# Kernel optimization log

Hardware: AMD Instinct MI355X
Metric: run time of the kernel (lower is better)

## Reference

```python
import jax, jax.numpy as jnp
import numpy as np

NEG_SLOPE = 0.2  # PyG GATConv default leaky_relu slope


def gat_conv(x, ei, W, a_src, a_dst, b, heads, ch):
    """One PyG-style GATConv (eval mode, add_self_loops already applied to ei)."""
    N = x.shape[0]
    h = (x @ W).reshape(N, heads, ch)                      # [N,H,C]
    src, dst = ei[0], ei[1]
    al_s = jnp.sum(h * a_src, axis=-1)                     # [N,H]
    al_d = jnp.sum(h * a_dst, axis=-1)                     # [N,H]
    e = jax.nn.leaky_relu(al_s[src] + al_d[dst], NEG_SLOPE)  # [E,H]
    m = jax.ops.segment_max(e, dst, num_segments=N)        # stable softmax over in-edges
    ex = jnp.exp(e - m[dst])
    den = jax.ops.segment_sum(ex, dst, num_segments=N)
    alpha = ex / den[dst]                                  # [E,H]
    msg = alpha[:, :, None] * h[src]                       # [E,H,C]
    out = jax.ops.segment_sum(msg, dst, num_segments=N)    # [N,H,C]
    return out.reshape(N, heads * ch) + b


def setup_inputs() -> dict:
    key = jax.random.key(0)
    ks = jax.random.split(key, 12)
    N, E, D_in, C, H, D_out = 10000, 320000, 256, 128, 4, 64
    HC = H * C

    def glorot(k, shape):
        fan = shape[0] + shape[-1]
        return jax.random.normal(k, shape, dtype=jnp.float32) * np.sqrt(2.0 / fan)

    x = jax.random.normal(ks[0], (N, D_in), dtype=jnp.float32)
    edge_index = jax.random.randint(ks[1], (2, E), 0, N, dtype=jnp.int64)
    return {
        "x": x,
        "edge_index": edge_index,
        "W1": glorot(ks[2], (D_in, HC)),
        "a_src1": glorot(ks[3], (H, C)),
        "a_dst1": glorot(ks[4], (H, C)),
        "b1": jnp.zeros((HC,), dtype=jnp.float32),
        "W2": glorot(ks[5], (HC, HC)),
        "a_src2": glorot(ks[6], (H, C)),
        "a_dst2": glorot(ks[7], (H, C)),
        "b2": jnp.zeros((HC,), dtype=jnp.float32),
        "W3": glorot(ks[8], (HC, D_out)),
        "a_src3": glorot(ks[9], (1, D_out)),
        "a_dst3": glorot(ks[10], (1, D_out)),
        "b3": jnp.zeros((D_out,), dtype=jnp.float32),
    }


def reference(x, edge_index, W1, a_src1, a_dst1, b1, W2, a_src2, a_dst2, b2,
              W3, a_src3, a_dst3, b3):
    N = x.shape[0]
    loops = jnp.arange(N, dtype=edge_index.dtype)
    ei = jnp.concatenate([edge_index, jnp.stack([loops, loops])], axis=1)
    H, C = a_src1.shape
    h = jax.nn.elu(gat_conv(x, ei, W1, a_src1, a_dst1, b1, H, C))
    h = jax.nn.elu(gat_conv(h, ei, W2, a_src2, a_dst2, b2, H, C))
    out = gat_conv(h, ei, W3, a_src3, a_dst3, b3, 1, a_src3.shape[1])
    return out
```

## Files before the change

kernel.cpp:

```cpp
#include <hip/hip_runtime.h>

typedef short bf16x8 __attribute__((ext_vector_type(8)));
typedef float f32x4 __attribute__((ext_vector_type(4)));

__device__ __forceinline__ unsigned short f2bf(float f) {
    unsigned u = __float_as_uint(f);
    unsigned r = (u + 0x7fffu + ((u >> 16) & 1u)) >> 16;
    return (unsigned short)r;
}
__device__ __forceinline__ float bf2f(unsigned short u) {
    return __uint_as_float(((unsigned)u) << 16);
}

__device__ __forceinline__ void gload_lds16(const void* g, void* l) {
    __builtin_amdgcn_global_load_lds(
        (const __attribute__((address_space(1))) unsigned int*)g,
        (__attribute__((address_space(3))) unsigned int*)l, 16, 0, 0);
}

__global__ void k_prep(const float* __restrict__ W1, unsigned short* __restrict__ W1T,
                       const float* __restrict__ W2, unsigned short* __restrict__ W2T,
                       const float* __restrict__ W3, unsigned short* __restrict__ W3T,
                       const float* __restrict__ x, unsigned short* __restrict__ xb,
                       int* __restrict__ csr, int Mcap,
                       const int* __restrict__ ei, int E, int* __restrict__ deg,
                       int DIN, int HC, int DOUT, int N)
{
    int i = blockIdx.x * blockDim.x + threadIdx.x;
    int n1 = DIN * HC;
    int n2 = n1 + HC * HC;
    int n3 = n2 + HC * DOUT;
    int n4 = n3 + N * DIN;
    int n5 = n4 + Mcap;
    int n6 = n5 + E;
    if (i < n1) {
        int k = i / HC, n = i - k * HC;
        W1T[n * DIN + k] = f2bf(W1[i]);
    } else if (i < n2) {
        int j = i - n1;
        int k = j / HC, n = j - k * HC;
        W2T[n * HC + k] = f2bf(W2[j]);
    } else if (i < n3) {
        int j = i - n2;
        int k = j / DOUT, n = j - k * DOUT;
        W3T[n * HC + k] = f2bf(W3[j]);
    } else if (i < n4) {
        int j = i - n3;
        xb[j] = f2bf(x[j]);
    } else if (i < n5) {
        csr[i - n4] = -1;
    } else if (i < n6) {
        atomicAdd(&deg[ei[E + (i - n5)]], 1);
    }
}

__global__ void k_scan(const int* __restrict__ deg, int* __restrict__ off,
                       int* __restrict__ cur, int N) {
    __shared__ int sums[1024];
    int t = threadIdx.x;
    int chunk = (N + 1023) >> 10;
    int lo = t * chunk;
    int hi = lo + chunk; if (hi > N) hi = N;
    if (lo > N) lo = N;
    int s = 0;
    for (int i = lo; i < hi; ++i) s += (deg[i] + 4) & ~3;
    sums[t] = s;
    __syncthreads();
    for (int dd = 1; dd < 1024; dd <<= 1) {
        int v = (t >= dd) ? sums[t - dd] : 0;
        __syncthreads();
        sums[t] += v;
        __syncthreads();
    }
    int run = sums[t] - s;
    for (int i = lo; i < hi; ++i) { off[i] = run; cur[i] = run; run += (deg[i] + 4) & ~3; }
    if (t == 1023) off[N] = run;
}
__global__ void k_fill(const int* __restrict__ ei, int E, int N,
                       int* cur, int* __restrict__ csr, int* __restrict__ dstarr) {
    int i = blockIdx.x * blockDim.x + threadIdx.x;
    if (i < E) {
        int s = ei[i], d = ei[E + i];
        int pos = atomicAdd(&cur[d], 1);
        csr[pos] = s;
        dstarr[pos] = d;
    } else if (i < E + N) {
        int nn = i - E;
        int pos = atomicAdd(&cur[nn], 1);
        csr[pos] = nn;
        dstarr[pos] = nn;
    }
}

template <bool OUTBF>
__global__ __launch_bounds__(256) void k_gemm(
    const unsigned short* __restrict__ A, const unsigned short* __restrict__ BT,
    void* __restrict__ D, int M, int K, int Nc, int tiles_n)
{
    int wid = blockIdx.x * (blockDim.x >> 6) + (threadIdx.x >> 6);
    int tiles_m = (M + 63) >> 6;
    if (wid >= tiles_m * tiles_n) return;
    int lane = threadIdx.x & 63;
    int tm = wid / tiles_n, tn = wid - tm * tiles_n;
    int m0 = tm << 6, n0 = tn << 6;
    int r = lane & 15, q = lane >> 4;

    const unsigned short* Arow[4];
    const unsigned short* Brow[4];
#pragma unroll
    for (int i = 0; i < 4; ++i) {
        int row = m0 + 16 * i + r; row = row < M ? row : M - 1;
        Arow[i] = A + (size_t)row * K + q * 8;
        Brow[i] = BT + (size_t)(n0 + 16 * i + r) * K + q * 8;
    }

    f32x4 acc[4][4] = {};
    bf16x8 a[4], b[4], a2[4], b2[4];
#pragma unroll
    for (int i = 0; i < 4; ++i) {
        a[i] = *(const bf16x8*)(Arow[i]);
        b[i] = *(const bf16x8*)(Brow[i]);
    }
    for (int k0 = 0; k0 < K; k0 += 32) {
        int kn = k0 + 32;
        if (kn < K) {
#pragma unroll
            for (int i = 0; i < 4; ++i) {
                a2[i] = *(const bf16x8*)(Arow[i] + kn);
                b2[i] = *(const bf16x8*)(Brow[i] + kn);
            }
        }
#pragma unroll
        for (int i = 0; i < 4; ++i)
#pragma unroll
            for (int j = 0; j < 4; ++j)
                acc[i][j] = __builtin_amdgcn_mfma_f32_16x16x32_bf16(a[i], b[j], acc[i][j], 0, 0, 0);
        if (kn < K) {
#pragma unroll
            for (int i = 0; i < 4; ++i) { a[i] = a2[i]; b[i] = b2[i]; }
        }
    }
#pragma unroll
    for (int i = 0; i < 4; ++i) {
        int rowb = m0 + 16 * i + q * 4;
#pragma unroll
        for (int rr = 0; rr < 4; ++rr) {
            int row = rowb + rr;
            if (row < M) {
#pragma unroll
                for (int j = 0; j < 4; ++j) {
                    int col = n0 + 16 * j + r;
                    if (OUTBF)
                        ((unsigned short*)D)[(size_t)row * Nc + col] = f2bf(acc[i][j][rr]);
                    else
                        ((float*)D)[(size_t)row * Nc + col] = acc[i][j][rr];
                }
            }
        }
    }
}

__global__ __launch_bounds__(256) void k_gemm_lds(
    const unsigned short* __restrict__ A, const unsigned short* __restrict__ BT,
    unsigned short* __restrict__ D, int M, int K, int Nc, int tiles_n)
{
    __shared__ unsigned short As[128 * 32];
    __shared__ unsigned short Bs[64 * 32];
    int tm = blockIdx.x / tiles_n, tn = blockIdx.x - tm * tiles_n;
    int m0 = tm << 7, n0 = tn << 6;
    int tid = threadIdx.x;
    int w = tid >> 6, lane = tid & 63;
    int wr = w >> 1, wc = w & 1;
    int r = lane & 15, q = lane >> 4;

    int lrow = lane >> 2;
    int lch = (lane & 3) * 8;
    int ga0 = m0 + w * 16 + lrow;       if (ga0 >= M) ga0 = M - 1;
    int ga1 = m0 + (w + 4) * 16 + lrow; if (ga1 >= M) ga1 = M - 1;
    const unsigned short* pa0 = A + (size_t)ga0 * K + lch;
    const unsigned short* pa1 = A + (size_t)ga1 * K + lch;
    const unsigned short* pb  = BT + (size_t)(n0 + w * 16 + lrow) * K + lch;
    unsigned short* lA0 = As + w * 512;
    unsigned short* lA1 = As + (w + 4) * 512;
    unsigned short* lB  = Bs + w * 512;

    const unsigned short* arp = As + (wr * 64 + r) * 32 + q * 8;
    const unsigned short* brp = Bs + (wc * 32 + r) * 32 + q * 8;

    f32x4 acc[4][2] = {};
    for (int k0 = 0; k0 < K; k0 += 32) {
        gload_lds16(pa0 + k0, lA0);
        gload_lds16(pa1 + k0, lA1);
        gload_lds16(pb + k0, lB);
        __syncthreads();
        bf16x8 a[4], b[2];
#pragma unroll
        for (int i = 0; i < 4; ++i) a[i] = *(const bf16x8*)(arp + i * 16 * 32);
#pragma unroll
        for (int j = 0; j < 2; ++j) b[j] = *(const bf16x8*)(brp + j * 16 * 32);
#pragma unroll
        for (int i = 0; i < 4; ++i)
#pragma unroll
            for (int j = 0; j < 2; ++j)
                acc[i][j] = __builtin_amdgcn_mfma_f32_16x16x32_bf16(a[i], b[j], acc[i][j], 0, 0, 0);
        __syncthreads();
    }
#pragma unroll
    for (int i = 0; i < 4; ++i) {
        int rowb = m0 + wr * 64 + 16 * i + q * 4;
#pragma unroll
        for (int rr = 0; rr < 4; ++rr) {
            int row = rowb + rr;
            if (row < M) {
#pragma unroll
                for (int j = 0; j < 2; ++j) {
                    int col = n0 + wc * 32 + 16 * j + r;
                    D[(size_t)row * Nc + col] = f2bf(acc[i][j][rr]);
                }
            }
        }
    }
}

template <int HCt, int Ht>
__global__ __launch_bounds__(256) void k_al(
    const unsigned short* __restrict__ h, const float* __restrict__ asrc,
    const float* __restrict__ adst,
    float* __restrict__ als, float* __restrict__ ald, int N)
{
    int wid = blockIdx.x * (blockDim.x >> 6) + (threadIdx.x >> 6);
    if (wid >= N) return;
    int lane = threadIdx.x & 63;
    const int CH = HCt / 64;
    const int Gs = 64 / Ht;
    float s = 0.f, d = 0.f;
    if constexpr (CH == 8) {
        const uint4* hr = (const uint4*)(h + (size_t)wid * HCt) + lane;
        uint4 hv = *hr;
        unsigned wds[4] = {hv.x, hv.y, hv.z, hv.w};
        const f32x4* as4 = (const f32x4*)(asrc + lane * 8);
        const f32x4* ad4 = (const f32x4*)(adst + lane * 8);
        f32x4 av0 = as4[0], av1 = as4[1], dv0 = ad4[0], dv1 = ad4[1];
        float hf[8];
#pragma unroll
        for (int wv = 0; wv < 4; ++wv) {
            hf[2 * wv]     = __uint_as_float(wds[wv] << 16);
            hf[2 * wv + 1] = __uint_as_float(wds[wv] & 0xffff0000u);
        }
#pragma unroll
        for (int j = 0; j < 4; ++j) {
            s += hf[j] * av0[j] + hf[4 + j] * av1[j];
            d += hf[j] * dv0[j] + hf[4 + j] * dv1[j];
        }
    } else {
        float hv = bf2f(h[(size_t)wid * HCt + lane]);
        s = hv * asrc[lane];
        d = hv * adst[lane];
    }
#pragma unroll
    for (int dd = 1; dd < Gs; dd <<= 1) {
        s += __shfl_xor(s, dd);
        d += __shfl_xor(d, dd);
    }
    if ((lane & (Gs - 1)) == 0) {
        int hh = lane / Gs;
        als[wid * Ht + hh] = s;
        ald[wid * Ht + hh] = d;
    }
}

__global__ void k_alpha4(const float* __restrict__ als, const float* __restrict__ ald,
                         const int* __restrict__ csr, const int* __restrict__ dstarr,
                         const int* __restrict__ off, int N,
                         float* __restrict__ alpha, int Mcap)
{
    int t = blockIdx.x * blockDim.x + threadIdx.x;
    if (t >= off[N]) return;
    int s = csr[t];
    if (s < 0) {
#pragma unroll
        for (int h = 0; h < 4; ++h) alpha[(size_t)h * Mcap + t] = 0.f;
        return;
    }
    int d = dstarr[t];
    f32x4 a = *(const f32x4*)(als + (size_t)s * 4);
    f32x4 b = *(const f32x4*)(ald + (size_t)d * 4);
#pragma unroll
    for (int h = 0; h < 4; ++h) {
        float l = a[h] + b[h];
        l = l > 0.f ? l : 0.2f * l;
        alpha[(size_t)h * Mcap + t] = __expf(l);
    }
}

template <bool DOELU>
__global__ __launch_bounds__(256) void k_aggr4b(
    const unsigned short* __restrict__ h, const float* __restrict__ alpha,
    const int* __restrict__ off, const int* __restrict__ csr,
    const float* __restrict__ bias,
    unsigned short* __restrict__ outp, int N, int nodeBlocks, int Mcap)
{
    int head = blockIdx.x / nodeBlocks;
    int nb = blockIdx.x - head * nodeBlocks;
    int n = nb * 4 + (threadIdx.x >> 6);
    if (n >= N) return;
    int lane = threadIdx.x & 63;
    int g = lane >> 4;
    int p = lane & 15;
    int q0 = (off[n] >> 2) + g, q1 = off[n + 1] >> 2;

    float acc[8] = {};
    float den = 0.f;
    const unsigned short* hbase = h + head * 128 + p * 8;
    const int4* csr4 = (const int4*)csr;
    const f32x4* al4 = (const f32x4*)(alpha + (size_t)head * Mcap);

    auto fmaq = [&](float a, const uint4& hq) {
        unsigned wds[4] = {hq.x, hq.y, hq.z, hq.w};
#pragma unroll
        for (int wv = 0; wv < 4; ++wv) {
            acc[2 * wv]     += a * __uint_as_float(wds[wv] << 16);
            acc[2 * wv + 1] += a * __uint_as_float(wds[wv] & 0xffff0000u);
        }
    };

    for (int q = q0; q < q1; q += 4) {
        int4 cs = csr4[q];
        f32x4 av = al4[q];
        int c0 = cs.x < 0 ? 0 : cs.x;
        int c1 = cs.y < 0 ? 0 : cs.y;
        int c2 = cs.z < 0 ? 0 : cs.z;
        int c3 = cs.w < 0 ? 0 : cs.w;
        uint4 h0 = *(const uint4*)(hbase + ((size_t)(unsigned)c0 << 9));
        uint4 h1 = *(const uint4*)(hbase + ((size_t)(unsigned)c1 << 9));
        uint4 h2 = *(const uint4*)(hbase + ((size_t)(unsigned)c2 << 9));
        uint4 h3 = *(const uint4*)(hbase + ((size_t)(unsigned)c3 << 9));
        den += (av[0] + av[1]) + (av[2] + av[3]);
        fmaq(av[0], h0);
        fmaq(av[1], h1);
        fmaq(av[2], h2);
        fmaq(av[3], h3);
    }

    den += __shfl_xor(den, 16);
    den += __shfl_xor(den, 32);
#pragma unroll
    for (int j = 0; j < 8; ++j) {
        acc[j] += __shfl_xor(acc[j], 16);
        acc[j] += __shfl_xor(acc[j], 32);
    }

    if (g == 0) {
        float inv = 1.f / den;
        int cb = head * 128 + p * 8;
        unsigned ww[4];
#pragma unroll
        for (int wv = 0; wv < 4; ++wv) {
            float v0 = acc[2 * wv] * inv + bias[cb + 2 * wv];
            float v1 = acc[2 * wv + 1] * inv + bias[cb + 2 * wv + 1];
            if (DOELU) {
                v0 = v0 > 0.f ? v0 : expm1f(v0);
                v1 = v1 > 0.f ? v1 : expm1f(v1);
            }
            ww[wv] = (unsigned)f2bf(v0) | ((unsigned)f2bf(v1) << 16);
        }
        uint4 o; o.x = ww[0]; o.y = ww[1]; o.z = ww[2]; o.w = ww[3];
        *((uint4*)(outp + (size_t)n * 512 + cb)) = o;
    }
}

__global__ __launch_bounds__(256) void k_aggr1b(
    const unsigned short* __restrict__ h, const float* __restrict__ als,
    const float* __restrict__ aldv, const int* __restrict__ off,
    const int* __restrict__ csr, const float* __restrict__ bias,
    float* __restrict__ outp, int N)
{
    int n = blockIdx.x * (blockDim.x >> 6) + (threadIdx.x >> 6);
    if (n >= N) return;
    int lane = threadIdx.x & 63;
    int g = lane >> 4;
    int p = lane & 15;
    int q0 = (off[n] >> 2) + g, q1 = off[n + 1] >> 2;
    float aldh = aldv[n];

    float acc[4] = {};
    float den = 0.f;
    const unsigned short* hbase = h + p * 4;
    const int4* csr4 = (const int4*)csr;

    auto aof = [&](int ss) -> float {
        int sc = ss < 0 ? 0 : ss;
        float l = als[sc] + aldh;
        l = l > 0.f ? l : 0.2f * l;
        float e = __expf(l);
        return ss < 0 ? 0.f : e;
    };
    auto fmaq = [&](float a, const uint2& hq) {
        den += a;
        acc[0] += a * __uint_as_float(hq.x << 16);
        acc[1] += a * __uint_as_float(hq.x & 0xffff0000u);
        acc[2] += a * __uint_as_float(hq.y << 16);
        acc[3] += a * __uint_as_float(hq.y & 0xffff0000u);
    };

    for (int q = q0; q < q1; q += 4) {
        int4 cs = csr4[q];
        float a0 = aof(cs.x), a1 = aof(cs.y), a2 = aof(cs.z), a3 = aof(cs.w);
        uint2 h0 = *(const uint2*)(hbase + ((size_t)(unsigned)(cs.x < 0 ? 0 : cs.x) << 6));
        uint2 h1 = *(const uint2*)(hbase + ((size_t)(unsigned)(cs.y < 0 ? 0 : cs.y) << 6));
        uint2 h2 = *(const uint2*)(hbase + ((size_t)(unsigned)(cs.z < 0 ? 0 : cs.z) << 6));
        uint2 h3 = *(const uint2*)(hbase + ((size_t)(unsigned)(cs.w < 0 ? 0 : cs.w) << 6));
        fmaq(a0, h0);
        fmaq(a1, h1);
        fmaq(a2, h2);
        fmaq(a3, h3);
    }

    den += __shfl_xor(den, 16);
    den += __shfl_xor(den, 32);
#pragma unroll
    for (int j = 0; j < 4; ++j) {
        acc[j] += __shfl_xor(acc[j], 16);
        acc[j] += __shfl_xor(acc[j], 32);
    }
    if (g == 0) {
        float inv = 1.f / den;
        f32x4 o;
#pragma unroll
        for (int j = 0; j < 4; ++j)
            o[j] = acc[j] * inv + bias[p * 4 + j];
        *((f32x4*)(outp + (size_t)n * 64 + p * 4)) = o;
    }
}

extern "C" void kernel_launch(void* const* d_in, const int* in_sizes, int n_in,
                              void* d_out, int out_size, void* d_ws, size_t ws_size,
                              hipStream_t stream)
{
    const float* x   = (const float*)d_in[0];
    const int*   ei  = (const int*)d_in[1];
    const float* W1  = (const float*)d_in[2];
    const float* as1 = (const float*)d_in[3];
    const float* ad1 = (const float*)d_in[4];
    const float* b1  = (const float*)d_in[5];
    const float* W2  = (const float*)d_in[6];
    const float* as2 = (const float*)d_in[7];
    const float* ad2 = (const float*)d_in[8];
    const float* b2  = (const float*)d_in[9];
    const float* W3  = (const float*)d_in[10];
    const float* as3 = (const float*)d_in[11];
    const float* ad3 = (const float*)d_in[12];
    const float* b3  = (const float*)d_in[13];

    const int DIN = 256, HC = 512, DOUT = 64;
    int N = in_sizes[0] / DIN;
    int E = in_sizes[1] / 2;
    int Mcap = E + 4 * N;

    char* w = (char*)d_ws;
    auto alloc = [&](size_t bytes) -> char* {
        char* p = w;
        w += (bytes + 255) & ~(size_t)255;
        return p;
    };
    int* deg    = (int*)alloc((size_t)N * 4);
    int* cur    = (int*)alloc((size_t)N * 4);
    int* off    = (int*)alloc((size_t)(N + 1) * 4);
    int* csr    = (int*)alloc((size_t)Mcap * 4);
    int* dstarr = (int*)alloc((size_t)Mcap * 4);
    unsigned short* W1T = (unsigned short*)alloc((size_t)HC * DIN * 2);
    unsigned short* W2T = (unsigned short*)alloc((size_t)HC * HC * 2);
    unsigned short* W3T = (unsigned short*)alloc((size_t)DOUT * HC * 2);
    unsigned short* xb  = (unsigned short*)alloc((size_t)N * DIN * 2);
    unsigned short* act = (unsigned short*)alloc((size_t)N * HC * 2);
    unsigned short* hb  = (unsigned short*)alloc((size_t)N * HC * 2);
    unsigned short* hb3 = (unsigned short*)alloc((size_t)N * DOUT * 2);
    float* als   = (float*)alloc((size_t)N * 4 * 4);
    float* ald   = (float*)alloc((size_t)N * 4 * 4);
    float* alpha = (float*)alloc((size_t)Mcap * 4 * 4);

    hipMemsetAsync(deg, 0, (size_t)N * 4, stream);
    int prep_total = DIN * HC + HC * HC + HC * DOUT + N * DIN + Mcap + E;
    k_prep<<<(prep_total + 255) / 256, 256, 0, stream>>>(
        W1, W1T, W2, W2T, W3, W3T, x, xb, csr, Mcap, ei, E, deg, DIN, HC, DOUT, N);
    k_scan<<<1, 1024, 0, stream>>>(deg, off, cur, N);
    k_fill<<<(E + N + 255) / 256, 256, 0, stream>>>(ei, E, N, cur, csr, dstarr);

    int tiles_m = (N + 63) / 64;
    auto gemm_blocks = [&](int tn) { return (tiles_m * tn + 3) / 4; };
    int tm128 = (N + 127) / 128;
    int nwave_blocks = (N + 3) / 4;
    int nodeBlocks = (N + 3) / 4;
    int alpha_blocks = (Mcap + 255) / 256;

    k_gemm_lds<<<tm128 * (HC / 64), 256, 0, stream>>>(xb, W1T, hb, N, DIN, HC, HC / 64);
    k_al<512, 4><<<nwave_blocks, 256, 0, stream>>>(hb, as1, ad1, als, ald, N);
    k_alpha4<<<alpha_blocks, 256, 0, stream>>>(als, ald, csr, dstarr, off, N, alpha, Mcap);
    k_aggr4b<true><<<4 * nodeBlocks, 256, 0, stream>>>(hb, alpha, off, csr, b1, act, N, nodeBlocks, Mcap);

    k_gemm_lds<<<tm128 * (HC / 64), 256, 0, stream>>>(act, W2T, hb, N, HC, HC, HC / 64);
    k_al<512, 4><<<nwave_blocks, 256, 0, stream>>>(hb, as2, ad2, als, ald, N);
    k_alpha4<<<alpha_blocks, 256, 0, stream>>>(als, ald, csr, dstarr, off, N, alpha, Mcap);
    k_aggr4b<true><<<4 * nodeBlocks, 256, 0, stream>>>(hb, alpha, off, csr, b2, act, N, nodeBlocks, Mcap);

    k_gemm<true><<<gemm_blocks(1), 256, 0, stream>>>(act, W3T, hb3, N, HC, DOUT, 1);
    k_al<64, 1><<<nwave_blocks, 256, 0, stream>>>(hb3, as3, ad3, als, ald, N);
    k_aggr1b<<<nwave_blocks, 256, 0, stream>>>(hb3, als, ald, off, csr, b3, (float*)d_out, N);
}
```

Baseline: 289.2 us.

## Switch bf16 storage and MFMA to fp16; fuse layer-3 attention logits into GEMM

Every bf16 conversion and bf16 MFMA is replaced by fp16 (`__half` conversions and `mfma_f32_16x16x32_f16`), and the aggregation and logit kernels now unpack with half2 intrinsics. Separately, the final small GEMM gains a DOAL path that computes the source and destination attention dot products from the fp32 accumulators with lane shuffles. That path removes the separate k_al launch for layer 3 and its reread of hb3. The fp16 switch trades bf16's wider exponent range for more mantissa bits, which risks overflow on large activations, and its half-to-float conversions may cost slightly more than the old shift-based bf16 unpack.

Result: no change. 294.5 us (+1.9%).

```diff
diff --git a/kernel.cpp b/kernel.cpp
--- a/kernel.cpp
+++ b/kernel.cpp
@@ -1,15 +1,16 @@
 #include <hip/hip_runtime.h>
-
-typedef short bf16x8 __attribute__((ext_vector_type(8)));
+#include <hip/hip_fp16.h>
+
+typedef _Float16 f16x8 __attribute__((ext_vector_type(8)));
 typedef float f32x4 __attribute__((ext_vector_type(4)));
 
-__device__ __forceinline__ unsigned short f2bf(float f) {
-    unsigned u = __float_as_uint(f);
-    unsigned r = (u + 0x7fffu + ((u >> 16) & 1u)) >> 16;
-    return (unsigned short)r;
-}
-__device__ __forceinline__ float bf2f(unsigned short u) {
-    return __uint_as_float(((unsigned)u) << 16);
+__device__ __forceinline__ unsigned short f2h_bits(float f) {
+    __half h = __float2half(f);
+    return *reinterpret_cast<unsigned short*>(&h);
+}
+__device__ __forceinline__ float h2f_bits(unsigned short u) {
+    __half h = *reinterpret_cast<__half*>(&u);
+    return __half2float(h);
 }
 
 __device__ __forceinline__ void gload_lds16(const void* g, void* l) {
@@ -35,18 +36,18 @@
     int n6 = n5 + E;
     if (i < n1) {
         int k = i / HC, n = i - k * HC;
-        W1T[n * DIN + k] = f2bf(W1[i]);
+        W1T[n * DIN + k] = f2h_bits(W1[i]);
     } else if (i < n2) {
         int j = i - n1;
         int k = j / HC, n = j - k * HC;
-        W2T[n * HC + k] = f2bf(W2[j]);
+        W2T[n * HC + k] = f2h_bits(W2[j]);
     } else if (i < n3) {
         int j = i - n2;
         int k = j / DOUT, n = j - k * DOUT;
-        W3T[n * HC + k] = f2bf(W3[j]);
+        W3T[n * HC + k] = f2h_bits(W3[j]);
     } else if (i < n4) {
         int j = i - n3;
-        xb[j] = f2bf(x[j]);
+        xb[j] = f2h_bits(x[j]);
     } else if (i < n5) {
         csr[i - n4] = -1;
     } else if (i < n6) {
@@ -92,10 +93,12 @@
     }
 }
 
-template <bool OUTBF>
+template <bool OUTH, bool DOAL>
 __global__ __launch_bounds__(256) void k_gemm(
     const unsigned short* __restrict__ A, const unsigned short* __restrict__ BT,
-    void* __restrict__ D, int M, int K, int Nc, int tiles_n)
+    void* __restrict__ D, int M, int K, int Nc, int tiles_n,
+    const float* __restrict__ asrc, const float* __restrict__ adst,
+    float* __restrict__ als, float* __restrict__ ald)
 {
     int wid = blockIdx.x * (blockDim.x >> 6) + (threadIdx.x >> 6);
     int tiles_m = (M + 63) >> 6;
@@ -115,26 +118,26 @@
     }
 
     f32x4 acc[4][4] = {};
-    bf16x8 a[4], b[4], a2[4], b2[4];
+    f16x8 a[4], b[4], a2[4], b2[4];
 #pragma unroll
     for (int i = 0; i < 4; ++i) {
-        a[i] = *(const bf16x8*)(Arow[i]);
-        b[i] = *(const bf16x8*)(Brow[i]);
+        a[i] = *(const f16x8*)(Arow[i]);
+        b[i] = *(const f16x8*)(Brow[i]);
     }
     for (int k0 = 0; k0 < K; k0 += 32) {
         int kn = k0 + 32;
         if (kn < K) {
 #pragma unroll
             for (int i = 0; i < 4; ++i) {
-                a2[i] = *(const bf16x8*)(Arow[i] + kn);
-                b2[i] = *(const bf16x8*)(Brow[i] + kn);
+                a2[i] = *(const f16x8*)(Arow[i] + kn);
+                b2[i] = *(const f16x8*)(Brow[i] + kn);
             }
         }
 #pragma unroll
         for (int i = 0; i < 4; ++i)
 #pragma unroll
             for (int j = 0; j < 4; ++j)
-                acc[i][j] = __builtin_amdgcn_mfma_f32_16x16x32_bf16(a[i], b[j], acc[i][j], 0, 0, 0);
+                acc[i][j] = __builtin_amdgcn_mfma_f32_16x16x32_f16(a[i], b[j], acc[i][j], 0, 0, 0);
         if (kn < K) {
 #pragma unroll
             for (int i = 0; i < 4; ++i) { a[i] = a2[i]; b[i] = b2[i]; }
@@ -150,11 +153,35 @@
 #pragma unroll
                 for (int j = 0; j < 4; ++j) {
                     int col = n0 + 16 * j + r;
-                    if (OUTBF)
-                        ((unsigned short*)D)[(size_t)row * Nc + col] = f2bf(acc[i][j][rr]);
+                    if (OUTH)
+                        ((unsigned short*)D)[(size_t)row * Nc + col] = f2h_bits(acc[i][j][rr]);
                     else
                         ((float*)D)[(size_t)row * Nc + col] = acc[i][j][rr];
                 }
+            }
+        }
+    }
+    if (DOAL) {
+        float asl[4], adl[4];
+#pragma unroll
+        for (int j = 0; j < 4; ++j) { asl[j] = asrc[16 * j + r]; adl[j] = adst[16 * j + r]; }
+#pragma unroll
+        for (int i = 0; i < 4; ++i) {
+#pragma unroll
+            for (int rr = 0; rr < 4; ++rr) {
+                float s = 0.f, d = 0.f;
+#pragma unroll
+                for (int j = 0; j < 4; ++j) {
+                    s += acc[i][j][rr] * asl[j];
+                    d += acc[i][j][rr] * adl[j];
+                }
+#pragma unroll
+                for (int dd = 1; dd < 16; dd <<= 1) {
+                    s += __shfl_xor(s, dd);
+                    d += __shfl_xor(d, dd);
+                }
+                int row = m0 + 16 * i + q * 4 + rr;
+                if (r == 0 && row < M) { als[row] = s; ald[row] = d; }
             }
         }
     }
@@ -193,16 +220,16 @@
         gload_lds16(pa1 + k0, lA1);
         gload_lds16(pb + k0, lB);
         __syncthreads();
-        bf16x8 a[4], b[2];
-#pragma unroll
-        for (int i = 0; i < 4; ++i) a[i] = *(const bf16x8*)(arp + i * 16 * 32);
-#pragma unroll
-        for (int j = 0; j < 2; ++j) b[j] = *(const bf16x8*)(brp + j * 16 * 32);
+        f16x8 a[4], b[2];
+#pragma unroll
+        for (int i = 0; i < 4; ++i) a[i] = *(const f16x8*)(arp + i * 16 * 32);
+#pragma unroll
+        for (int j = 0; j < 2; ++j) b[j] = *(const f16x8*)(brp + j * 16 * 32);
 #pragma unroll
         for (int i = 0; i < 4; ++i)
 #pragma unroll
             for (int j = 0; j < 2; ++j)
-                acc[i][j] = __builtin_amdgcn_mfma_f32_16x16x32_bf16(a[i], b[j], acc[i][j], 0, 0, 0);
+                acc[i][j] = __builtin_amdgcn_mfma_f32_16x16x32_f16(a[i], b[j], acc[i][j], 0, 0, 0);
         __syncthreads();
     }
 #pragma unroll
@@ -215,7 +242,7 @@
 #pragma unroll
                 for (int j = 0; j < 2; ++j) {
                     int col = n0 + wc * 32 + 16 * j + r;
-                    D[(size_t)row * Nc + col] = f2bf(acc[i][j][rr]);
+                    D[(size_t)row * Nc + col] = f2h_bits(acc[i][j][rr]);
                 }
             }
         }
@@ -241,19 +268,19 @@
         const f32x4* as4 = (const f32x4*)(asrc + lane * 8);
         const f32x4* ad4 = (const f32x4*)(adst + lane * 8);
         f32x4 av0 = as4[0], av1 = as4[1], dv0 = ad4[0], dv1 = ad4[1];
-        float hf[8];
 #pragma unroll
         for (int wv = 0; wv < 4; ++wv) {
-            hf[2 * wv]     = __uint_as_float(wds[wv] << 16);
-            hf[2 * wv + 1] = __uint_as_float(wds[wv] & 0xffff0000u);
-        }
-#pragma unroll
-        for (int j = 0; j < 4; ++j) {
-            s += hf[j] * av0[j] + hf[4 + j] * av1[j];
-            d += hf[j] * dv0[j] + hf[4 + j] * dv1[j];
+            __half2 p = *reinterpret_cast<const __half2*>(&wds[wv]);
+            float h0 = __low2float(p), h1 = __high2float(p);
+            float a0 = (wv < 2) ? av0[2 * wv] : av1[2 * (wv - 2)];
+            float a1 = (wv < 2) ? av0[2 * wv + 1] : av1[2 * (wv - 2) + 1];
+            float d0 = (wv < 2) ? dv0[2 * wv] : dv1[2 * (wv - 2)];
+            float d1 = (wv < 2) ? dv0[2 * wv + 1] : dv1[2 * (wv - 2) + 1];
+            s = fmaf(h0, a0, s); s = fmaf(h1, a1, s);
+            d = fmaf(h0, d0, d); d = fmaf(h1, d1, d);
         }
     } else {
-        float hv = bf2f(h[(size_t)wid * HCt + lane]);
+        float hv = h2f_bits(h[(size_t)wid * HCt + lane]);
         s = hv * asrc[lane];
         d = hv * adst[lane];
     }
@@ -319,8 +346,9 @@
         unsigned wds[4] = {hq.x, hq.y, hq.z, hq.w};
 #pragma unroll
         for (int wv = 0; wv < 4; ++wv) {
-            acc[2 * wv]     += a * __uint_as_float(wds[wv] << 16);
-            acc[2 * wv + 1] += a * __uint_as_float(wds[wv] & 0xffff0000u);
+            __half2 pp = *reinterpret_cast<const __half2*>(&wds[wv]);
+            acc[2 * wv]     = fmaf(a, __low2float(pp),  acc[2 * wv]);
+            acc[2 * wv + 1] = fmaf(a, __high2float(pp), acc[2 * wv + 1]);
         }
     };
 
@@ -362,7 +390,7 @@
                 v0 = v0 > 0.f ? v0 : expm1f(v0);
                 v1 = v1 > 0.f ? v1 : expm1f(v1);
             }
-            ww[wv] = (unsigned)f2bf(v0) | ((unsigned)f2bf(v1) << 16);
+            ww[wv] = (unsigned)f2h_bits(v0) | ((unsigned)f2h_bits(v1) << 16);
         }
         uint4 o; o.x = ww[0]; o.y = ww[1]; o.z = ww[2]; o.w = ww[3];
         *((uint4*)(outp + (size_t)n * 512 + cb)) = o;
@@ -397,10 +425,12 @@
     };
     auto fmaq = [&](float a, const uint2& hq) {
         den += a;
-        acc[0] += a * __uint_as_float(hq.x << 16);
-        acc[1] += a * __uint_as_float(hq.x & 0xffff0000u);
-        acc[2] += a * __uint_as_float(hq.y << 16);
-        acc[3] += a * __uint_as_float(hq.y & 0xffff0000u);
+        __half2 p0 = *reinterpret_cast<const __half2*>(&hq.x);
+        __half2 p1 = *reinterpret_cast<const __half2*>(&hq.y);
+        acc[0] = fmaf(a, __low2float(p0),  acc[0]);
+        acc[1] = fmaf(a, __high2float(p0), acc[1]);
+        acc[2] = fmaf(a, __low2float(p1),  acc[2]);
+        acc[3] = fmaf(a, __high2float(p1), acc[3]);
     };
 
     for (int q = q0; q < q1; q += 4) {
@@ -503,7 +533,7 @@
     k_alpha4<<<alpha_blocks, 256, 0, stream>>>(als, ald, csr, dstarr, off, N, alpha, Mcap);
     k_aggr4b<true><<<4 * nodeBlocks, 256, 0, stream>>>(hb, alpha, off, csr, b2, act, N, nodeBlocks, Mcap);
 
-    k_gemm<true><<<gemm_blocks(1), 256, 0, stream>>>(act, W3T, hb3, N, HC, DOUT, 1);
-    k_al<64, 1><<<nwave_blocks, 256, 0, stream>>>(hb3, as3, ad3, als, ald, N);
+    k_gemm<true, true><<<gemm_blocks(1), 256, 0, stream>>>(
+        act, W3T, hb3, N, HC, DOUT, 1, as3, ad3, als, ald);
     k_aggr1b<<<nwave_blocks, 256, 0, stream>>>(hb3, als, ald, off, csr, b3, (float*)d_out, N);
 }
```
